# Optimization experiments

Measured on AMD Instinct MI355X. Metric: run time of the kernel, lower is better.

## Reference

```python
import jax, jax.numpy as jnp
import numpy as np

N_LOW = 50000
N_HIGH = 200000
E = 1000000       # number of (i, j, k) triplets from the radius search
K = 27            # 3x3x3 voxel kernel cells
C_IN = 128
C_OUT = 128


def setup_inputs() -> dict:
    key = jax.random.key(0)
    k0, k1, k2, k3, k4, k5 = jax.random.split(key, 6)
    x_low = jax.random.normal(k0, (N_LOW, C_IN), dtype=jnp.float32)
    # PointConv3d weight: one [C_OUT, C_IN] matrix per kernel cell, kaiming-ish scale
    weight = jax.random.normal(k1, (K, C_OUT, C_IN), dtype=jnp.float32) * (1.0 / np.sqrt(C_IN))
    bias = jax.random.normal(k2, (C_OUT,), dtype=jnp.float32) * 0.01
    i_high = jax.random.randint(k3, (E,), 0, N_HIGH, dtype=jnp.int32)
    j_low = jax.random.randint(k4, (E,), 0, N_LOW, dtype=jnp.int32)
    k_cell = jax.random.randint(k5, (E,), 0, K, dtype=jnp.int32)
    return {"x_low": x_low, "weight": weight, "bias": bias,
            "i_high": i_high, "j_low": j_low, "k": k_cell, "n_high": N_HIGH}


def reference(x_low, weight, bias, i_high, j_low, k, n_high):
    # Sparse point convolution: out[i] += weight[k] @ x_low[j], then + bias.
    # Efficient form: transform every low-res point by all K kernel matrices once
    # (dense GEMM), then gather the (j, k) entry per triplet and scatter-add by i.
    y = jnp.einsum('nc,koc->nko', x_low, weight)       # [N_low, K, C_out]
    msg = y[j_low, k]                                  # [E, C_out] gather
    out = jnp.zeros((n_high, weight.shape[1]), dtype=x_low.dtype)
    out = out.at[i_high].add(msg)                      # scatter-add to high-res points
    return out + bias
```

## Files before the change

### kernel.cpp

```cpp
#include <hip/hip_runtime.h>

typedef _Float16 half8 __attribute__((ext_vector_type(8)));
typedef _Float16 half4v __attribute__((ext_vector_type(4)));
typedef _Float16 half2v __attribute__((ext_vector_type(2)));
typedef float f32x4 __attribute__((ext_vector_type(4)));

#define CAP 32
#define OVF_MAX 4096


__global__ void cvt_inputs(const float* __restrict__ x, const float* __restrict__ w,
                           const float* __restrict__ bias,
                           _Float16* __restrict__ Xh, _Float16* __restrict__ Wh,
                           float* __restrict__ biasPerm,
                           int xv4, int xt4, int w4) {
    int i = blockIdx.x * blockDim.x + threadIdx.x;
    if (i < xt4) {
        float4 v = (i < xv4) ? reinterpret_cast<const float4*>(x)[i]
                             : make_float4(0.f, 0.f, 0.f, 0.f);
        half4v h; h[0]=(_Float16)v.x; h[1]=(_Float16)v.y; h[2]=(_Float16)v.z; h[3]=(_Float16)v.w;
        reinterpret_cast<half4v*>(Xh)[i] = h;
    } else if (i < xt4 + w4) {
        int j = i - xt4;
        float4 v = reinterpret_cast<const float4*>(w)[j];
        half4v h; h[0]=(_Float16)v.x; h[1]=(_Float16)v.y; h[2]=(_Float16)v.z; h[3]=(_Float16)v.w;
        reinterpret_cast<half4v*>(Wh)[j] = h;
    } else if (i < xt4 + w4 + 32) {
        int j2 = i - xt4 - w4;
        int wn = j2 >> 4, mrow = j2 & 15;
        float4 v;
        v.x = bias[wn * 64 + 0 * 16 + mrow];
        v.y = bias[wn * 64 + 1 * 16 + mrow];
        v.z = bias[wn * 64 + 2 * 16 + mrow];
        v.w = bias[wn * 64 + 3 * 16 + mrow];
        reinterpret_cast<float4*>(biasPerm)[j2] = v;
    }
}

__global__ void zero_ints(int* __restrict__ p, int n) {
    int i = blockIdx.x * blockDim.x + threadIdx.x;
    if (i < n) p[i] = 0;
}

__global__ void init_bias(float* __restrict__ out, const float* __restrict__ bias, int n4) {
    int i = blockIdx.x * blockDim.x + threadIdx.x;
    if (i >= n4) return;
    reinterpret_cast<float4*>(out)[i] = reinterpret_cast<const float4*>(bias)[i & 31];
}

__global__ __launch_bounds__(256) void fill_buckets(
    const int* __restrict__ ih, const int* __restrict__ jl, const int* __restrict__ kc,
    int* __restrict__ counts, int* __restrict__ bucket,
    int* __restrict__ ovf_cnt, int* __restrict__ ovf_list,
    unsigned* __restrict__ mask, int Mpad,
    int E, int ldY) {
    int e = blockIdx.x * blockDim.x + threadIdx.x;
    if (e >= E) return;
    int i = ih[e];
    int j = jl[e], kk = kc[e];
    int cell = kk * Mpad + j;
    atomicOr(&mask[cell >> 5], 1u << (cell & 31));
    int off = j * ldY + kk * 128;
    int pos = atomicAdd(&counts[i], 1);
    if (pos < CAP) {
        bucket[(size_t)i * CAP + pos] = off;
    } else {
        int o = atomicAdd(ovf_cnt, 1);
        if (o < OVF_MAX) { ovf_list[2 * o] = i; ovf_list[2 * o + 1] = off; }
    }
}

__global__ __launch_bounds__(256) void gemm_xw(
    const _Float16* __restrict__ Xh,
    const _Float16* __restrict__ Wh,
    _Float16* __restrict__ Y,
    const unsigned* __restrict__ mask,
    int Mpad, int ldY) {
    __shared__ ushort sA[128 * 128];
    __shared__ ushort sB[128 * 128];
    const int tid = threadIdx.x;
    const int m0 = blockIdx.x * 128;
    const int kc0 = blockIdx.y * 3;
    const ushort* Ag = (const ushort*)Xh + (size_t)m0 * 128;

#pragma unroll
    for (int it = 0; it < 8; ++it) {
        int p = it * 256 + tid;
        int row = p >> 4, cpos = p & 15;
        int csrc = cpos ^ (row & 15);
        __builtin_amdgcn_global_load_lds(
            (const __attribute__((address_space(1))) void*)(Ag + row * 128 + csrc * 8),
            (__attribute__((address_space(3))) void*)(&sA[row * 128 + cpos * 8]), 16, 0, 0);
    }
    {
        const ushort* Bg = (const ushort*)Wh + (size_t)kc0 * 128 * 128;
#pragma unroll
        for (int it = 0; it < 8; ++it) {
            int p = it * 256 + tid;
            int row = p >> 4, cpos = p & 15;
            int csrc = cpos ^ (row & 15);
            __builtin_amdgcn_global_load_lds(
                (const __attribute__((address_space(1))) void*)(Bg + row * 128 + csrc * 8),
                (__attribute__((address_space(3))) void*)(&sB[row * 128 + cpos * 8]), 16, 0, 0);
        }
    }
    __builtin_amdgcn_s_waitcnt(0);
    __syncthreads();

    const int lane = tid & 63;
    const int wid = tid >> 6;
    const int wm = wid & 1, wn = wid >> 1;
    const int mrow = lane & 15;
    const int g = lane >> 4;

    for (int kk = 0; kk < 3; ++kk) {
        f32x4 acc[4][4] = {};
#pragma unroll
        for (int kb = 0; kb < 4; ++kb) {
            half8 af[4], bf[4];
#pragma unroll
            for (int t = 0; t < 4; ++t) {
                int cpos8 = ((kb * 4 + g) ^ mrow) * 8;
                int ra = wm * 64 + t * 16 + mrow;
                af[t] = *reinterpret_cast<const half8*>(&sA[ra * 128 + cpos8]);
                int rb = wn * 64 + t * 16 + mrow;
                bf[t] = *reinterpret_cast<const half8*>(&sB[rb * 128 + cpos8]);
            }
#pragma unroll
            for (int mt = 0; mt < 4; ++mt)
#pragma unroll
                for (int nt = 0; nt < 4; ++nt)
                    acc[mt][nt] = __builtin_amdgcn_mfma_f32_16x16x32_f16(
                        af[mt], bf[nt], acc[mt][nt], 0, 0, 0);
        }
        __syncthreads();
        if (kk < 2) {
            const ushort* Bg = (const ushort*)Wh + (size_t)(kc0 + kk + 1) * 128 * 128;
#pragma unroll
            for (int it = 0; it < 8; ++it) {
                int p = it * 256 + tid;
                int row = p >> 4, cpos = p & 15;
                int csrc = cpos ^ (row & 15);
                __builtin_amdgcn_global_load_lds(
                    (const __attribute__((address_space(1))) void*)(Bg + row * 128 + csrc * 8),
                    (__attribute__((address_space(3))) void*)(&sB[row * 128 + cpos * 8]), 16, 0, 0);
            }
        }
        const unsigned* mwp = mask + (((size_t)(kc0 + kk) * Mpad + m0) >> 5);
        unsigned mw0 = mwp[0], mw1 = mwp[1], mw2 = mwp[2], mw3 = mwp[3];
        unsigned mAsel = wm ? mw2 : mw0;
        unsigned mBsel = wm ? mw3 : mw1;
        _Float16* Yt = Y + (size_t)m0 * ldY + (kc0 + kk) * 128 + wn * 64 + mrow * 4;
#pragma unroll
        for (int mt = 0; mt < 4; ++mt) {
            unsigned msel = (mt < 2) ? mAsel : mBsel;
#pragma unroll
            for (int r = 0; r < 4; ++r) {
                int bit = (mt & 1) * 16 + g * 4 + r;
                if ((msel >> bit) & 1u) {
                    int row = wm * 64 + mt * 16 + g * 4 + r;
                    half4v hv;
#pragma unroll
                    for (int nt = 0; nt < 4; ++nt) hv[nt] = (_Float16)acc[mt][nt][r];
                    *reinterpret_cast<half4v*>(Yt + (size_t)row * ldY) = hv;
                }
            }
        }
        if (kk < 2) {
            __builtin_amdgcn_s_waitcnt(0);
            __syncthreads();
        }
    }
}

__global__ __launch_bounds__(256) void gather_out(
    const _Float16* __restrict__ Y, const int* __restrict__ counts,
    const int* __restrict__ bucket, const float* __restrict__ biasPerm,
    float* __restrict__ out, int Nhigh, int zoff) {
    int wave = (blockIdx.x * blockDim.x + threadIdx.x) >> 6;
    int lane = threadIdx.x & 63;
    int p = lane >> 4;
    int sub = lane & 15;
    int i = wave * 4 + p;
    bool act = i < Nhigh;
    int iC = act ? i : 0;
    int nb = counts[iC];
    if (nb > CAP) nb = CAP;
    const int* bk = bucket + (size_t)iC * CAP;
    int offsA = bk[sub];
    int offsB = bk[sub + 16];
    float4 b0 = reinterpret_cast<const float4*>(biasPerm)[sub * 2];
    float4 b1 = reinterpret_cast<const float4*>(biasPerm)[sub * 2 + 1];
    float acc[8] = {b0.x, b0.y, b0.z, b0.w, b1.x, b1.y, b1.z, b1.w};

    int nmax = nb;
    nmax = max(nmax, __shfl_xor(nmax, 16));
    nmax = max(nmax, __shfl_xor(nmax, 32));

    for (int e0 = 0; e0 < nmax; e0 += 4) {
#pragma unroll
        for (int u = 0; u < 4; ++u) {
            int e = e0 + u;
            int off = (e < 16) ? __shfl(offsA, p * 16 + (e & 15))
                               : __shfl(offsB, p * 16 + (e & 15));
            bool valid = act && (e < nb);
            off = valid ? off : zoff;
            half8 h = *reinterpret_cast<const half8*>(Y + (size_t)off + sub * 8);
#pragma unroll
            for (int t = 0; t < 8; ++t) acc[t] += (float)h[t];
        }
    }
    if (act) {
        float* op = out + (size_t)i * 128;
        int obase = (sub >> 3) * 64 + (sub & 7) * 2;
#pragma unroll
        for (int t = 0; t < 8; ++t)
            op[obase + (t & 3) * 16 + (t >> 2)] = acc[t];
    }
}

__global__ void apply_overflow(const int* __restrict__ ovf_cnt, const int* __restrict__ ovf_list,
                               const _Float16* __restrict__ Y, float* __restrict__ out) {
    int n = *ovf_cnt;
    if (n > OVF_MAX) n = OVF_MAX;
    int lane = threadIdx.x & 63;
    int w = threadIdx.x >> 6;
    int o0p = 2 * lane, o1p = 2 * lane + 1;
    int o0 = (o0p >> 6) * 64 + (o0p & 3) * 16 + ((o0p >> 2) & 15);
    int o1 = (o1p >> 6) * 64 + (o1p & 3) * 16 + ((o1p >> 2) & 15);
    for (int o = w; o < n; o += 4) {
        int i = ovf_list[2 * o], off = ovf_list[2 * o + 1];
        half2v h = *reinterpret_cast<const half2v*>(Y + (size_t)off + lane * 2);
        float* dst = out + (size_t)i * 128;
        unsafeAtomicAdd(dst + o0, (float)h[0]);
        unsafeAtomicAdd(dst + o1, (float)h[1]);
    }
}

__global__ void fallback_edge(const float* __restrict__ x, const float* __restrict__ w,
                              const int* __restrict__ ih, const int* __restrict__ jl,
                              const int* __restrict__ kc, float* __restrict__ out, int E) {
    int e = blockIdx.x;
    if (e >= E) return;
    int lane = threadIdx.x;
    int i = ih[e], j = jl[e], k = kc[e];
    const float* xr = x + (size_t)j * 128;
    const float* wk = w + (size_t)k * 128 * 128;
    float s0 = 0.f, s1 = 0.f;
    for (int c = 0; c < 128; ++c) {
        float xv = xr[c];
        s0 += wk[(size_t)lane * 128 + c] * xv;
        s1 += wk[(size_t)(lane + 64) * 128 + c] * xv;
    }
    unsafeAtomicAdd(&out[(size_t)i * 128 + lane], s0);
    unsafeAtomicAdd(&out[(size_t)i * 128 + 64 + lane], s1);
}

extern "C" void kernel_launch(void* const* d_in, const int* in_sizes, int n_in,
                              void* d_out, int out_size, void* d_ws, size_t ws_size,
                              hipStream_t stream) {
    const float* x    = (const float*)d_in[0];
    const float* w    = (const float*)d_in[1];
    const float* bias = (const float*)d_in[2];
    const int*   ih   = (const int*)d_in[3];
    const int*   jl   = (const int*)d_in[4];
    const int*   kc   = (const int*)d_in[5];
    float* out = (float*)d_out;

    const int C = 128;
    const int Nlow = in_sizes[0] / C;
    const int K = in_sizes[1] / (C * C);
    const int E = in_sizes[3];
    const int ldY = K * C;
    const int Nhigh = out_size / C;

    const int mtiles = (Nlow + 127) / 128;
    const int Mpad = mtiles * 128;
    const int maskwords = (Mpad * K + 31) / 32;

    size_t off = 0;
    auto alloc = [&](size_t bytes) { size_t o = off; off = (off + bytes + 255) & ~(size_t)255; return o; };
    size_t xh_off   = alloc((size_t)Mpad * C * 2);
    size_t wh_off   = alloc((size_t)K * C * C * 2);
    size_t bp_off   = alloc((size_t)C * 4);
    size_t cnt_off  = alloc(((size_t)Nhigh + 1 + maskwords) * 4);
    size_t ovl_off  = alloc((size_t)OVF_MAX * 2 * 4);
    size_t bkt_off  = alloc((size_t)Nhigh * CAP * 4);
    size_t y_off    = alloc(((size_t)Mpad * ldY + C) * 2);
    size_t need_sort = off;

    _Float16* Xh = (_Float16*)((char*)d_ws + xh_off);
    _Float16* Wh = (_Float16*)((char*)d_ws + wh_off);
    float* biasPerm = (float*)((char*)d_ws + bp_off);
    int* counts  = (int*)((char*)d_ws + cnt_off);
    int* ovf_cnt = counts + Nhigh;
    unsigned* mask = (unsigned*)(counts + Nhigh + 1);
    int* ovf_lst = (int*)((char*)d_ws + ovl_off);
    int* bucket  = (int*)((char*)d_ws + bkt_off);
    _Float16* Y  = (_Float16*)((char*)d_ws + y_off);
    const int zoff = Mpad * ldY;

    if (ws_size >= need_sort && (K % 3) == 0) {
        int xv4 = Nlow * C / 4, xt4 = Mpad * C / 4;
        int w4 = K * C * C / 4;
        cvt_inputs<<<(xt4 + w4 + 32 + 255) / 256, 256, 0, stream>>>(
            x, w, bias, Xh, Wh, biasPerm, xv4, xt4, w4);
        int nz = Nhigh + 1 + maskwords;
        zero_ints<<<(nz + 255) / 256, 256, 0, stream>>>(counts, nz);
        zero_ints<<<1, 64, 0, stream>>>((int*)(Y + (size_t)zoff), C / 2);
        fill_buckets<<<(E + 255) / 256, 256, 0, stream>>>(
            ih, jl, kc, counts, bucket, ovf_cnt, ovf_lst, mask, Mpad, E, ldY);
        gemm_xw<<<dim3(mtiles, K / 3), 256, 0, stream>>>(Xh, Wh, Y, mask, Mpad, ldY);
        gather_out<<<(Nhigh + 15) / 16, 256, 0, stream>>>(
            Y, counts, bucket, biasPerm, out, Nhigh, zoff);
        apply_overflow<<<1, 256, 0, stream>>>(ovf_cnt, ovf_lst, Y, out);
    } else {
        int n4out = out_size / 4;
        init_bias<<<(n4out + 255) / 256, 256, 0, stream>>>(out, bias, n4out);
        fallback_edge<<<E, 64, 0, stream>>>(x, w, ih, jl, kc, out, E);
    }
}
```

Measured before the change: 389.4 us.

## Use byte mask with plain stores and fuse bucket fill into GEMM prologue

The old fill_buckets kernel did both the mask atomicOr and the bucketing atomics. It is split in two. A light mask_store kernel now writes one byte per (k, j) cell with ordinary stores instead of bit atomics. The bucket-filling atomics move into the gemm_xw prologue, where they run while the async global-to-LDS loads are in flight. This aims to hide the atomic scatter latency behind the GEMM loads and to cut atomic contention on the mask, at the cost of a larger mask buffer and extra work in the GEMM blocks.

```diff
diff --git a/kernel.cpp b/kernel.cpp
--- a/kernel.cpp
+++ b/kernel.cpp
@@ -48,34 +48,24 @@
     reinterpret_cast<float4*>(out)[i] = reinterpret_cast<const float4*>(bias)[i & 31];
 }
 
-__global__ __launch_bounds__(256) void fill_buckets(
-    const int* __restrict__ ih, const int* __restrict__ jl, const int* __restrict__ kc,
-    int* __restrict__ counts, int* __restrict__ bucket,
-    int* __restrict__ ovf_cnt, int* __restrict__ ovf_list,
-    unsigned* __restrict__ mask, int Mpad,
-    int E, int ldY) {
+__global__ __launch_bounds__(256) void mask_store(
+    const int* __restrict__ jl, const int* __restrict__ kc,
+    unsigned char* __restrict__ maskB, int Mpad, int E) {
     int e = blockIdx.x * blockDim.x + threadIdx.x;
     if (e >= E) return;
-    int i = ih[e];
-    int j = jl[e], kk = kc[e];
-    int cell = kk * Mpad + j;
-    atomicOr(&mask[cell >> 5], 1u << (cell & 31));
-    int off = j * ldY + kk * 128;
-    int pos = atomicAdd(&counts[i], 1);
-    if (pos < CAP) {
-        bucket[(size_t)i * CAP + pos] = off;
-    } else {
-        int o = atomicAdd(ovf_cnt, 1);
-        if (o < OVF_MAX) { ovf_list[2 * o] = i; ovf_list[2 * o + 1] = off; }
-    }
+    maskB[(size_t)kc[e] * Mpad + jl[e]] = 1;
 }
 
 __global__ __launch_bounds__(256) void gemm_xw(
     const _Float16* __restrict__ Xh,
     const _Float16* __restrict__ Wh,
     _Float16* __restrict__ Y,
-    const unsigned* __restrict__ mask,
-    int Mpad, int ldY) {
+    const unsigned char* __restrict__ maskB,
+    int Mpad, int ldY,
+    const int* __restrict__ ih, const int* __restrict__ jl,
+    const int* __restrict__ kc,
+    int* __restrict__ counts, int* __restrict__ bucket,
+    int* __restrict__ ovf_cnt, int* __restrict__ ovf_list, int E) {
     __shared__ ushort sA[128 * 128];
     __shared__ ushort sB[128 * 128];
     const int tid = threadIdx.x;
@@ -104,6 +94,26 @@
                 (__attribute__((address_space(3))) void*)(&sB[row * 128 + cpos * 8]), 16, 0, 0);
         }
     }
+
+    {
+        int nb = gridDim.x * gridDim.y;
+        int bid = blockIdx.y * gridDim.x + blockIdx.x;
+        int per = (E + nb - 1) / nb;
+        int e0 = bid * per;
+        int e1 = e0 + per; if (e1 > E) e1 = E;
+        for (int e = e0 + tid; e < e1; e += 256) {
+            int i = ih[e];
+            int off = jl[e] * ldY + kc[e] * 128;
+            int pos = atomicAdd(&counts[i], 1);
+            if (pos < CAP) {
+                bucket[(size_t)i * CAP + pos] = off;
+            } else {
+                int o = atomicAdd(ovf_cnt, 1);
+                if (o < OVF_MAX) { ovf_list[2 * o] = i; ovf_list[2 * o + 1] = off; }
+            }
+        }
+    }
+
     __builtin_amdgcn_s_waitcnt(0);
     __syncthreads();
 
@@ -146,23 +156,21 @@
                     (__attribute__((address_space(3))) void*)(&sB[row * 128 + cpos * 8]), 16, 0, 0);
             }
         }
-        const unsigned* mwp = mask + (((size_t)(kc0 + kk) * Mpad + m0) >> 5);
-        unsigned mw0 = mwp[0], mw1 = mwp[1], mw2 = mwp[2], mw3 = mwp[3];
-        unsigned mAsel = wm ? mw2 : mw0;
-        unsigned mBsel = wm ? mw3 : mw1;
+        const unsigned char* mBp = maskB + (size_t)(kc0 + kk) * Mpad + m0 + wm * 64;
         _Float16* Yt = Y + (size_t)m0 * ldY + (kc0 + kk) * 128 + wn * 64 + mrow * 4;
 #pragma unroll
         for (int mt = 0; mt < 4; ++mt) {
-            unsigned msel = (mt < 2) ? mAsel : mBsel;
-#pragma unroll
-            for (int r = 0; r < 4; ++r) {
-                int bit = (mt & 1) * 16 + g * 4 + r;
-                if ((msel >> bit) & 1u) {
-                    int row = wm * 64 + mt * 16 + g * 4 + r;
-                    half4v hv;
-#pragma unroll
-                    for (int nt = 0; nt < 4; ++nt) hv[nt] = (_Float16)acc[mt][nt][r];
-                    *reinterpret_cast<half4v*>(Yt + (size_t)row * ldY) = hv;
+            unsigned mw = *reinterpret_cast<const unsigned*>(mBp + mt * 16 + g * 4);
+            if (mw) {
+#pragma unroll
+                for (int r = 0; r < 4; ++r) {
+                    if ((mw >> (8 * r)) & 0xFFu) {
+                        int row = wm * 64 + mt * 16 + g * 4 + r;
+                        half4v hv;
+#pragma unroll
+                        for (int nt = 0; nt < 4; ++nt) hv[nt] = (_Float16)acc[mt][nt][r];
+                        *reinterpret_cast<half4v*>(Yt + (size_t)row * ldY) = hv;
+                    }
                 }
             }
         }
@@ -276,14 +284,13 @@
 
     const int mtiles = (Nlow + 127) / 128;
     const int Mpad = mtiles * 128;
-    const int maskwords = (Mpad * K + 31) / 32;
 
     size_t off = 0;
     auto alloc = [&](size_t bytes) { size_t o = off; off = (off + bytes + 255) & ~(size_t)255; return o; };
     size_t xh_off   = alloc((size_t)Mpad * C * 2);
     size_t wh_off   = alloc((size_t)K * C * C * 2);
     size_t bp_off   = alloc((size_t)C * 4);
-    size_t cnt_off  = alloc(((size_t)Nhigh + 1 + maskwords) * 4);
+    size_t cnt_off  = alloc(((size_t)Nhigh + 1) * 4 + (size_t)Mpad * K);
     size_t ovl_off  = alloc((size_t)OVF_MAX * 2 * 4);
     size_t bkt_off  = alloc((size_t)Nhigh * CAP * 4);
     size_t y_off    = alloc(((size_t)Mpad * ldY + C) * 2);
@@ -294,7 +301,7 @@
     float* biasPerm = (float*)((char*)d_ws + bp_off);
     int* counts  = (int*)((char*)d_ws + cnt_off);
     int* ovf_cnt = counts + Nhigh;
-    unsigned* mask = (unsigned*)(counts + Nhigh + 1);
+    unsigned char* maskB = (unsigned char*)(counts + Nhigh + 1);
     int* ovf_lst = (int*)((char*)d_ws + ovl_off);
     int* bucket  = (int*)((char*)d_ws + bkt_off);
     _Float16* Y  = (_Float16*)((char*)d_ws + y_off);
@@ -305,12 +312,13 @@
         int w4 = K * C * C / 4;
         cvt_inputs<<<(xt4 + w4 + 32 + 255) / 256, 256, 0, stream>>>(
             x, w, bias, Xh, Wh, biasPerm, xv4, xt4, w4);
-        int nz = Nhigh + 1 + maskwords;
+        int nz = Nhigh + 1 + (Mpad * K) / 4;
         zero_ints<<<(nz + 255) / 256, 256, 0, stream>>>(counts, nz);
         zero_ints<<<1, 64, 0, stream>>>((int*)(Y + (size_t)zoff), C / 2);
-        fill_buckets<<<(E + 255) / 256, 256, 0, stream>>>(
-            ih, jl, kc, counts, bucket, ovf_cnt, ovf_lst, mask, Mpad, E, ldY);
-        gemm_xw<<<dim3(mtiles, K / 3), 256, 0, stream>>>(Xh, Wh, Y, mask, Mpad, ldY);
+        mask_store<<<(E + 255) / 256, 256, 0, stream>>>(jl, kc, maskB, Mpad, E);
+        gemm_xw<<<dim3(mtiles, K / 3), 256, 0, stream>>>(
+            Xh, Wh, Y, maskB, Mpad, ldY,
+            ih, jl, kc, counts, bucket, ovf_cnt, ovf_lst, E);
         gather_out<<<(Nhigh + 15) / 16, 256, 0, stream>>>(
             Y, counts, bucket, biasPerm, out, Nhigh, zoff);
         apply_overflow<<<1, 256, 0, stream>>>(ovf_cnt, ovf_lst, Y, out);
```

New measurement: 354.6 us. 8.9% less time.
